# Performance work log

Hardware: AMD Instinct MI355X
Metric: run time of the kernel (lower is better)

Reference implementation:

```python
import jax, jax.numpy as jnp
import numpy as np

NUM_EXPERTS = 16
HIDDEN = 2048
INTER = 768
TOP_K = 8
N_TOKENS = 4096


def setup_inputs() -> dict:
    key = jax.random.key(0)
    k1, k2, k3, k4, k5 = jax.random.split(key, 5)
    hidden_states = jax.random.normal(k1, (N_TOKENS, HIDDEN), dtype=jnp.float32)
    routing_weights = jax.random.uniform(k2, (N_TOKENS, NUM_EXPERTS), dtype=jnp.float32)
    router_indices = jax.random.randint(k3, (N_TOKENS, TOP_K), 0, NUM_EXPERTS)
    gate_up_proj = jax.random.normal(k4, (NUM_EXPERTS, HIDDEN, 2 * INTER), dtype=jnp.float32) * 0.02
    down_proj = jax.random.normal(k5, (NUM_EXPERTS, INTER, HIDDEN), dtype=jnp.float32) * 0.02
    return {
        "hidden_states": hidden_states,
        "routing_weights": routing_weights,
        "router_indices": router_indices,
        "gate_up_proj": gate_up_proj,
        "down_proj": down_proj,
    }


def reference(hidden_states, routing_weights, router_indices, gate_up_proj, down_proj):
    # Training-path MoE math (permute + grouped GEMM + SwiGLU + grouped GEMM +
    # unpermute/combine), expressed as dense per-expert GEMMs combined with a
    # sparse combine matrix built from the top-k router indices.
    n_tokens, hidden = hidden_states.shape
    n_experts = gate_up_proj.shape[0]
    # selected_probs[t, k] = routing_weights[t, router_indices[t, k]]
    selected_probs = jnp.take_along_axis(routing_weights, router_indices, axis=1)  # [N, K]
    # combine[t, e] = sum over k of selected_probs where router_indices[t,k] == e
    rows = jnp.arange(n_tokens)[:, None]
    combine = jnp.zeros((n_tokens, n_experts), dtype=hidden_states.dtype)
    combine = combine.at[rows, router_indices].add(selected_probs)  # [N, E]
    # grouped GEMM #1 (gate_up): [N,H] x [E,H,2I] -> [E,N,2I]
    gate_up = jnp.einsum("nh,ehf->enf", hidden_states, gate_up_proj)
    gate, up = jnp.split(gate_up, 2, axis=-1)
    inter = jax.nn.silu(gate) * up  # SwiGLU, [E,N,I]
    # grouped GEMM #2 (down): [E,N,I] x [E,I,H] -> [E,N,H]
    expert_out = jnp.einsum("eni,eih->enh", inter, down_proj)
    # combine / unpermute: weighted sum over selected experts
    out = jnp.einsum("enh,ne->nh", expert_out, combine)  # [N, H]
    return out
```

## Files before the change

kernel.cpp:

```cpp
#include <hip/hip_runtime.h>
#include <hip/hip_bf16.h>

#define NE 16
#define H  2048
#define I  768
#define TK 8
#define NT 4096
#define BM 128
#define BK 64

typedef unsigned short u16;
typedef unsigned int u32;
typedef __attribute__((ext_vector_type(8))) short bf16x8;
typedef __attribute__((ext_vector_type(4))) float f32x4;

__device__ __forceinline__ u16 f2bf(float f) {
    u32 u = __float_as_uint(f);
    u32 r = (u + 0x7fffu + ((u >> 16) & 1u)) >> 16;
    return (u16)r;
}

__device__ __forceinline__ void gload16(const void* g, void* l) {
    __builtin_amdgcn_global_load_lds(
        (const __attribute__((address_space(1))) unsigned int*)g,
        (__attribute__((address_space(3))) unsigned int*)l, 16, 0, 0);
}

__global__ void route_kernel(const float* __restrict__ rw, const int* __restrict__ ridx,
                             int* __restrict__ cnt, int* __restrict__ tok_cap,
                             float* __restrict__ wt_cap) {
    int t = blockIdx.x * 256 + threadIdx.x;
    if (t >= NT) return;
    int idx[TK];
#pragma unroll
    for (int k = 0; k < TK; k++) idx[k] = ridx[t * TK + k];
#pragma unroll
    for (int e = 0; e < NE; e++) {
        int mult = 0;
#pragma unroll
        for (int k = 0; k < TK; k++) mult += (idx[k] == e) ? 1 : 0;
        if (mult) {
            float w = (float)mult * rw[t * NE + e];
            int slot = atomicAdd(&cnt[e], 1);
            tok_cap[e * NT + slot] = t;
            wt_cap[e * NT + slot] = w;
        }
    }
}

__global__ void prefix_kernel(const int* __restrict__ cnt, int* __restrict__ base) {
    if (threadIdx.x == 0 && blockIdx.x == 0) {
        int s = 0;
        for (int e = 0; e < NE; e++) { base[e] = s; s += cnt[e]; }
        base[NE] = s;
    }
}

__global__ void compact_kernel(const int* __restrict__ cnt, const int* __restrict__ base,
                               const int* __restrict__ tok_cap, const float* __restrict__ wt_cap,
                               int* __restrict__ tok, float* __restrict__ wt,
                               int* __restrict__ tjc, int* __restrict__ tslot) {
    int i = blockIdx.x * 256 + threadIdx.x;
    int e = i >> 12, s = i & 4095;
    if (e < NE && s < cnt[e]) {
        int t = tok_cap[e * NT + s];
        int slot = base[e] + s;
        tok[slot] = t;
        wt[slot]  = wt_cap[e * NT + s];
        int j = atomicAdd(&tjc[t], 1);
        tslot[t * TK + j] = slot;
    }
}

__global__ void cvt_hs(const float4* __restrict__ in, uint4* __restrict__ out, int n) {
    int i = blockIdx.x * 256 + threadIdx.x;
    if (i >= n) return;
    float4 a = in[i * 2], b = in[i * 2 + 1];
    uint4 o;
    o.x = (u32)f2bf(a.x) | ((u32)f2bf(a.y) << 16);
    o.y = (u32)f2bf(a.z) | ((u32)f2bf(a.w) << 16);
    o.z = (u32)f2bf(b.x) | ((u32)f2bf(b.y) << 16);
    o.w = (u32)f2bf(b.z) | ((u32)f2bf(b.w) << 16);
    out[i] = o;
}

__global__ void transpose_cvt(const float* __restrict__ in, u32* __restrict__ out,
                              int K, int N) {
    __shared__ float tile[64][65];
    const float* src = in + (size_t)blockIdx.z * K * N;
    u32* dst = out + (size_t)blockIdx.z * (size_t)K * N / 2;
    int n0 = blockIdx.x * 64, k0 = blockIdx.y * 64;
    int tc = threadIdx.x & 63, tr = threadIdx.x >> 6;
    for (int r = tr; r < 64; r += 4)
        tile[r][tc] = src[(size_t)(k0 + r) * N + n0 + tc];
    __syncthreads();
    int kp = threadIdx.x & 31, rr = threadIdx.x >> 5;
    for (int r = rr; r < 64; r += 8) {
        u32 v = (u32)f2bf(tile[kp * 2][r]) | ((u32)f2bf(tile[kp * 2 + 1][r]) << 16);
        dst[(size_t)(n0 + r) * (K / 2) + k0 / 2 + kp] = v;
    }
}

__global__ __launch_bounds__(256, 2) void gemm1_kernel(
    const u16* __restrict__ hsb, const u16* __restrict__ w1t, u16* __restrict__ inter,
    const int* __restrict__ tok, const int* __restrict__ cnt, const int* __restrict__ base) {
    int bid = blockIdx.x;
    int lid = (bid & 7) * (6144 / 8) + (bid >> 3);
    int mt = lid & 31, r2 = lid >> 5;
    int nt = r2 % 12, e = r2 / 12;
    int cn = cnt[e];
    if (mt * BM >= cn) return;
    int b0 = base[e];

    __shared__ u16 lA[BM * BK];
    __shared__ u16 lB[BM * BK];

    int tid = threadIdx.x, lane = tid & 63, wv = tid >> 6;

    const u16* gA[4];
    const u16* gB[4];
#pragma unroll
    for (int i = 0; i < 4; i++) {
        int c = i * 256 + tid;
        int r = c >> 3, ko = (c & 7) * 8;
        int rg = mt * BM + r;
        int t = tok[b0 + min(rg, cn - 1)];
        gA[i] = hsb + (size_t)t * H + ko;
        int nrow = (r < 64) ? (nt * 64 + r) : (704 + nt * 64 + r);
        gB[i] = w1t + (size_t)e * 1536 * H + (size_t)nrow * H + ko;
    }
    u16* lAd[4];
    u16* lBd[4];
#pragma unroll
    for (int i = 0; i < 4; i++) {
        lAd[i] = lA + (i * 256 + wv * 64) * 8;
        lBd[i] = lB + (i * 256 + wv * 64) * 8;
    }

    f32x4 acc[2][8];
#pragma unroll
    for (int m = 0; m < 2; m++)
#pragma unroll
        for (int n = 0; n < 8; n++) acc[m][n] = (f32x4)0.0f;

    for (int kt = 0; kt < H / BK; ++kt) {
        __syncthreads();
#pragma unroll
        for (int i = 0; i < 4; i++) { gload16(gA[i], lAd[i]); gload16(gB[i], lBd[i]); }
#pragma unroll
        for (int i = 0; i < 4; i++) { gA[i] += BK; gB[i] += BK; }
        __syncthreads();
#pragma unroll
        for (int s = 0; s < 2; s++) {
            int kk = s * 32 + (lane >> 4) * 8;
            bf16x8 a0 = *(const bf16x8*)&lA[(wv * 32 + (lane & 15)) * BK + kk];
            bf16x8 a1 = *(const bf16x8*)&lA[(wv * 32 + 16 + (lane & 15)) * BK + kk];
#pragma unroll
            for (int n = 0; n < 8; n++) {
                bf16x8 b = *(const bf16x8*)&lB[(n * 16 + (lane & 15)) * BK + kk];
                acc[0][n] = __builtin_amdgcn_mfma_f32_16x16x32_bf16(a0, b, acc[0][n], 0, 0, 0);
                acc[1][n] = __builtin_amdgcn_mfma_f32_16x16x32_bf16(a1, b, acc[1][n], 0, 0, 0);
            }
        }
    }

    int jr = (lane >> 4) * 4, col = lane & 15;
#pragma unroll
    for (int m = 0; m < 2; m++)
#pragma unroll
        for (int j = 0; j < 4; j++) {
            int r = wv * 32 + m * 16 + jr + j;
            int rg = mt * BM + r;
            if (rg < cn) {
                size_t slot = (size_t)(b0 + rg);
#pragma unroll
                for (int n = 0; n < 4; n++) {
                    float g = acc[m][n][j];
                    float u = acc[m][n + 4][j];
                    float sv = g / (1.0f + __expf(-g)) * u;
                    inter[slot * I + nt * 64 + n * 16 + col] = f2bf(sv);
                }
            }
        }
}

template <int MODE>
__global__ __launch_bounds__(256, 2) void gemm2_kernel(
    const u16* __restrict__ inter, const u16* __restrict__ w2t,
    u16* __restrict__ eo, float* __restrict__ out,
    const int* __restrict__ tok, const float* __restrict__ wt,
    const int* __restrict__ cnt, const int* __restrict__ base) {
    int bid = blockIdx.x;
    int lid = (bid & 7) * (8192 / 8) + (bid >> 3);
    int mt = lid & 31, r2 = lid >> 5;
    int nt = r2 & 15, e = r2 >> 4;
    int cn = cnt[e];
    if (mt * BM >= cn) return;
    int b0 = base[e];

    __shared__ u16 lA[BM * BK];
    __shared__ u16 lB[BM * BK];

    int tid = threadIdx.x, lane = tid & 63, wv = tid >> 6;

    const u16* gA[4];
    const u16* gB[4];
#pragma unroll
    for (int i = 0; i < 4; i++) {
        int c = i * 256 + tid;
        int r = c >> 3, ko = (c & 7) * 8;
        gA[i] = inter + (size_t)(b0 + mt * BM + r) * I + ko;
        gB[i] = w2t + (size_t)e * H * I + (size_t)(nt * BM + r) * I + ko;
    }
    u16* lAd[4];
    u16* lBd[4];
#pragma unroll
    for (int i = 0; i < 4; i++) {
        lAd[i] = lA + (i * 256 + wv * 64) * 8;
        lBd[i] = lB + (i * 256 + wv * 64) * 8;
    }

    f32x4 acc[2][8];
#pragma unroll
    for (int m = 0; m < 2; m++)
#pragma unroll
        for (int n = 0; n < 8; n++) acc[m][n] = (f32x4)0.0f;

    for (int kt = 0; kt < I / BK; ++kt) {
        __syncthreads();
#pragma unroll
        for (int i = 0; i < 4; i++) { gload16(gA[i], lAd[i]); gload16(gB[i], lBd[i]); }
#pragma unroll
        for (int i = 0; i < 4; i++) { gA[i] += BK; gB[i] += BK; }
        __syncthreads();
#pragma unroll
        for (int s = 0; s < 2; s++) {
            int kk = s * 32 + (lane >> 4) * 8;
            bf16x8 a0 = *(const bf16x8*)&lA[(wv * 32 + (lane & 15)) * BK + kk];
            bf16x8 a1 = *(const bf16x8*)&lA[(wv * 32 + 16 + (lane & 15)) * BK + kk];
#pragma unroll
            for (int n = 0; n < 8; n++) {
                bf16x8 b = *(const bf16x8*)&lB[(n * 16 + (lane & 15)) * BK + kk];
                acc[0][n] = __builtin_amdgcn_mfma_f32_16x16x32_bf16(a0, b, acc[0][n], 0, 0, 0);
                acc[1][n] = __builtin_amdgcn_mfma_f32_16x16x32_bf16(a1, b, acc[1][n], 0, 0, 0);
            }
        }
    }

    int jr = (lane >> 4) * 4, col = lane & 15;
#pragma unroll
    for (int m = 0; m < 2; m++)
#pragma unroll
        for (int j = 0; j < 4; j++) {
            int r = wv * 32 + m * 16 + jr + j;
            int rg = mt * BM + r;
            if (rg < cn) {
                if (MODE == 0) {
                    u16* row = eo + (size_t)(b0 + rg) * H + nt * BM;
#pragma unroll
                    for (int n = 0; n < 8; n++)
                        row[n * 16 + col] = f2bf(acc[m][n][j]);
                } else {
                    int t = tok[b0 + rg];
                    float w = wt[b0 + rg];
                    float* orow = out + (size_t)t * H + nt * BM;
#pragma unroll
                    for (int n = 0; n < 8; n++)
                        atomicAdd(&orow[n * 16 + col], w * acc[m][n][j]);
                }
            }
        }
}

__global__ __launch_bounds__(256) void combine_kernel(
    const u16* __restrict__ eo, const float* __restrict__ wt,
    const int* __restrict__ tjc, const int* __restrict__ tslot,
    float* __restrict__ out) {
    int t = blockIdx.x;
    int c = threadIdx.x * 8;
    float acc[8];
#pragma unroll
    for (int i = 0; i < 8; i++) acc[i] = 0.0f;
    int jc = tjc[t];
    for (int j = 0; j < jc; j++) {
        int slot = tslot[t * TK + j];
        float w = wt[slot];
        uint4 v = *(const uint4*)(eo + (size_t)slot * H + c);
        acc[0] += w * __uint_as_float(v.x << 16);
        acc[1] += w * __uint_as_float(v.x & 0xffff0000u);
        acc[2] += w * __uint_as_float(v.y << 16);
        acc[3] += w * __uint_as_float(v.y & 0xffff0000u);
        acc[4] += w * __uint_as_float(v.z << 16);
        acc[5] += w * __uint_as_float(v.z & 0xffff0000u);
        acc[6] += w * __uint_as_float(v.w << 16);
        acc[7] += w * __uint_as_float(v.w & 0xffff0000u);
    }
    float4* o = (float4*)(out + (size_t)t * H + c);
    o[0] = make_float4(acc[0], acc[1], acc[2], acc[3]);
    o[1] = make_float4(acc[4], acc[5], acc[6], acc[7]);
}

extern "C" void kernel_launch(void* const* d_in, const int* in_sizes, int n_in,
                              void* d_out, int out_size, void* d_ws, size_t ws_size,
                              hipStream_t stream) {
    const float* hs  = (const float*)d_in[0];
    const float* rw  = (const float*)d_in[1];
    const int*   ri  = (const int*)d_in[2];
    const float* w1  = (const float*)d_in[3];
    const float* w2  = (const float*)d_in[4];
    float* out = (float*)d_out;

    char* ws = (char*)d_ws;
    size_t o = 0;
    auto alloc = [&](size_t bytes) { void* p = ws + o; o += (bytes + 255) & ~(size_t)255; return p; };
    int*   tokcap = (int*)alloc((size_t)NE * NT * 4);
    float* wtcap  = (float*)alloc((size_t)NE * NT * 4);
    int*   tok    = (int*)alloc((size_t)NT * TK * 4);
    float* wt     = (float*)alloc((size_t)NT * TK * 4);
    int*   tjc    = (int*)alloc((size_t)NT * 4);
    int*   tslot  = (int*)alloc((size_t)NT * TK * 4);
    int*   cnt    = (int*)alloc(64);
    int*   base   = (int*)alloc(128);
    u16*   hsb    = (u16*)alloc((size_t)NT * H * 2);
    u16*   w1t    = (u16*)alloc((size_t)NE * 1536 * H * 2);
    u16*   w2t    = (u16*)alloc((size_t)NE * H * I * 2);
    u16*   inter  = (u16*)alloc((size_t)(NT * TK + 256) * I * 2);
    u16*   eo     = (u16*)alloc((size_t)(NT * TK + 256) * H * 2);
    const bool use_eo = (o <= ws_size);

    hipMemsetAsync(cnt, 0, 64, stream);
    hipMemsetAsync(tjc, 0, (size_t)NT * 4, stream);
    if (!use_eo)
        hipMemsetAsync(out, 0, (size_t)NT * H * 4, stream);

    route_kernel<<<NT / 256, 256, 0, stream>>>(rw, ri, cnt, tokcap, wtcap);
    prefix_kernel<<<1, 64, 0, stream>>>(cnt, base);
    compact_kernel<<<NE * NT / 256, 256, 0, stream>>>(cnt, base, tokcap, wtcap, tok, wt, tjc, tslot);
    cvt_hs<<<(NT * H / 8 + 255) / 256, 256, 0, stream>>>((const float4*)hs, (uint4*)hsb, NT * H / 8);
    {
        dim3 g(1536 / 64, H / 64, NE);
        transpose_cvt<<<g, 256, 0, stream>>>(w1, (u32*)w1t, H, 1536);
    }
    {
        dim3 g(H / 64, I / 64, NE);
        transpose_cvt<<<g, 256, 0, stream>>>(w2, (u32*)w2t, I, H);
    }
    gemm1_kernel<<<6144, 256, 0, stream>>>(hsb, w1t, inter, tok, cnt, base);
    if (use_eo) {
        gemm2_kernel<0><<<8192, 256, 0, stream>>>(inter, w2t, eo, out, tok, wt, cnt, base);
        combine_kernel<<<NT, 256, 0, stream>>>(eo, wt, tjc, tslot, out);
    } else {
        gemm2_kernel<1><<<8192, 256, 0, stream>>>(inter, w2t, eo, out, tok, wt, cnt, base);
    }
}
```

Before: 801.8 us.

## Rewrite grouped GEMMs as 256x256 tiles with pipelined, swizzled LDS staging

Both grouped GEMMs move from 128x128 tiles with 256 threads and single-buffered LDS to 256x256 tiles with 512 threads (8 waves). K is staged in 32-wide chunks through a multi-buffered LDS ring using XOR-swizzled rows, with explicit vmcnt/lgkmcnt waits, barriers and MFMA priority hints, so global loads overlap with MFMA work. The atomic fallback path is dropped and the eo+combine path is always used. The larger tiles improve data reuse and cut synchronisation stalls, at the cost of 128KB of LDS per block, more padding waste on partially filled expert tiles, and heavier register pressure.

```diff
diff --git a/kernel.cpp b/kernel.cpp
--- a/kernel.cpp
+++ b/kernel.cpp
@@ -6,8 +6,6 @@
 #define I  768
 #define TK 8
 #define NT 4096
-#define BM 128
-#define BK 64
 
 typedef unsigned short u16;
 typedef unsigned int u32;
@@ -25,6 +23,87 @@
         (const __attribute__((address_space(1))) unsigned int*)g,
         (__attribute__((address_space(3))) unsigned int*)l, 16, 0, 0);
 }
+
+__device__ __forceinline__ void BAR() {
+    __builtin_amdgcn_sched_barrier(0);
+    __builtin_amdgcn_s_barrier();
+    __builtin_amdgcn_sched_barrier(0);
+}
+__device__ __forceinline__ void WLDS() {
+    asm volatile("s_waitcnt lgkmcnt(0)" ::: "memory");
+    __builtin_amdgcn_sched_barrier(0);
+}
+#define VM4() asm volatile("s_waitcnt vmcnt(4)" ::: "memory")
+
+#define MF(a, b, c) __builtin_amdgcn_mfma_f32_16x16x32_bf16(a, b, c, 0, 0, 0)
+
+#define FRAG(REG, ROW) (*(const bf16x8*)((REG) + (ROW)*32 + ((q ^ ((((ROW) >> 1)) & 3)) * 8)))
+
+#define STG(PR0, PR1, DST, KO)                       \
+    do {                                             \
+        gload16((PR0) + (KO), (DST) + tid * 8);      \
+        gload16((PR1) + (KO), (DST) + 4096 + tid * 8); \
+    } while (0)
+
+#define MFMA_Q(MH)                                                                     \
+    do {                                                                               \
+        acc[(MH)*4+0][0]=MF(af0,bf0,acc[(MH)*4+0][0]); acc[(MH)*4+0][1]=MF(af0,bf1,acc[(MH)*4+0][1]); \
+        acc[(MH)*4+0][2]=MF(af0,bf2,acc[(MH)*4+0][2]); acc[(MH)*4+0][3]=MF(af0,bf3,acc[(MH)*4+0][3]); \
+        acc[(MH)*4+1][0]=MF(af1,bf0,acc[(MH)*4+1][0]); acc[(MH)*4+1][1]=MF(af1,bf1,acc[(MH)*4+1][1]); \
+        acc[(MH)*4+1][2]=MF(af1,bf2,acc[(MH)*4+1][2]); acc[(MH)*4+1][3]=MF(af1,bf3,acc[(MH)*4+1][3]); \
+        acc[(MH)*4+2][0]=MF(af2,bf0,acc[(MH)*4+2][0]); acc[(MH)*4+2][1]=MF(af2,bf1,acc[(MH)*4+2][1]); \
+        acc[(MH)*4+2][2]=MF(af2,bf2,acc[(MH)*4+2][2]); acc[(MH)*4+2][3]=MF(af2,bf3,acc[(MH)*4+2][3]); \
+        acc[(MH)*4+3][0]=MF(af3,bf0,acc[(MH)*4+3][0]); acc[(MH)*4+3][1]=MF(af3,bf1,acc[(MH)*4+3][1]); \
+        acc[(MH)*4+3][2]=MF(af3,bf2,acc[(MH)*4+3][2]); acc[(MH)*4+3][3]=MF(af3,bf3,acc[(MH)*4+3][3]); \
+    } while (0)
+
+#define KTILE(cA0, cA1, cB0, cB1, oA1, oB1, T1, T2)                           \
+    do {                                                                      \
+        af0 = FRAG(cA0, wm*128 +  0 + ln); af1 = FRAG(cA0, wm*128 + 16 + ln); \
+        af2 = FRAG(cA0, wm*128 + 32 + ln); af3 = FRAG(cA0, wm*128 + 48 + ln); \
+        bf0 = FRAG(cB0, wn*64 +  0 + ln);  bf1 = FRAG(cB0, wn*64 + 16 + ln);  \
+        bf2 = FRAG(cB0, wn*64 + 32 + ln);  bf3 = FRAG(cB0, wn*64 + 48 + ln);  \
+        STG(pA0, pA1, oA1, (T1)*64 + 32);                                     \
+        BAR(); WLDS();                                                        \
+        __builtin_amdgcn_s_setprio(1); MFMA_Q(0); __builtin_amdgcn_s_setprio(0); \
+        BAR();                                                                \
+        af0 = FRAG(cA0, wm*128 + 64 + ln); af1 = FRAG(cA0, wm*128 + 80 + ln); \
+        af2 = FRAG(cA0, wm*128 + 96 + ln); af3 = FRAG(cA0, wm*128 +112 + ln); \
+        STG(pB0, pB1, oB1, (T1)*64 + 32);                                     \
+        BAR(); WLDS();                                                        \
+        __builtin_amdgcn_s_setprio(1); MFMA_Q(1); __builtin_amdgcn_s_setprio(0); \
+        BAR();                                                                \
+        af0 = FRAG(cA1, wm*128 +  0 + ln); af1 = FRAG(cA1, wm*128 + 16 + ln); \
+        af2 = FRAG(cA1, wm*128 + 32 + ln); af3 = FRAG(cA1, wm*128 + 48 + ln); \
+        bf0 = FRAG(cB1, wn*64 +  0 + ln);  bf1 = FRAG(cB1, wn*64 + 16 + ln);  \
+        bf2 = FRAG(cB1, wn*64 + 32 + ln);  bf3 = FRAG(cB1, wn*64 + 48 + ln);  \
+        STG(pA0, pA1, cA0, (T2)*64);                                          \
+        BAR(); WLDS();                                                        \
+        __builtin_amdgcn_s_setprio(1); MFMA_Q(0); __builtin_amdgcn_s_setprio(0); \
+        BAR();                                                                \
+        af0 = FRAG(cA1, wm*128 + 64 + ln); af1 = FRAG(cA1, wm*128 + 80 + ln); \
+        af2 = FRAG(cA1, wm*128 + 96 + ln); af3 = FRAG(cA1, wm*128 +112 + ln); \
+        STG(pB0, pB1, cB0, (T2)*64);                                          \
+        VM4();                                                                \
+        BAR(); WLDS();                                                        \
+        __builtin_amdgcn_s_setprio(1); MFMA_Q(1); __builtin_amdgcn_s_setprio(0); \
+        BAR();                                                                \
+    } while (0)
+
+#define GEMM_PRO_AND_DECLS()                                                  \
+    u16* const sA00 = sm;         u16* const sA01 = sm + 8192;                \
+    u16* const sA10 = sm + 16384; u16* const sA11 = sm + 24576;               \
+    u16* const sB00 = sm + 32768; u16* const sB01 = sm + 40960;               \
+    u16* const sB10 = sm + 49152; u16* const sB11 = sm + 57344;               \
+    f32x4 acc[8][4];                                                          \
+    _Pragma("unroll") for (int _i = 0; _i < 8; _i++)                          \
+    _Pragma("unroll") for (int _j = 0; _j < 4; _j++) acc[_i][_j] = (f32x4)0.0f; \
+    bf16x8 af0, af1, af2, af3, bf0, bf1, bf2, bf3;                            \
+     \
+    STG(pA0, pA1, sA00, 0);  STG(pB0, pB1, sB00, 0);                          \
+    STG(pA0, pA1, sA01, 32); STG(pB0, pB1, sB01, 32);                         \
+    STG(pA0, pA1, sA10, 64); STG(pB0, pB1, sB10, 64);                         \
+    VM4(); BAR();
 
 __global__ void route_kernel(const float* __restrict__ rw, const int* __restrict__ ridx,
                              int* __restrict__ cnt, int* __restrict__ tok_cap,
@@ -101,175 +180,113 @@
     }
 }
 
-__global__ __launch_bounds__(256, 2) void gemm1_kernel(
+__global__ __launch_bounds__(512, 2) void gemm1_kernel(
     const u16* __restrict__ hsb, const u16* __restrict__ w1t, u16* __restrict__ inter,
     const int* __restrict__ tok, const int* __restrict__ cnt, const int* __restrict__ base) {
+    __shared__ u16 sm[65536];
     int bid = blockIdx.x;
-    int lid = (bid & 7) * (6144 / 8) + (bid >> 3);
-    int mt = lid & 31, r2 = lid >> 5;
-    int nt = r2 % 12, e = r2 / 12;
+    int lid = (bid & 7) * (1536 / 8) + (bid >> 3);
+    int mt = lid & 15;
+    int r2 = lid >> 4;
+    int nt = r2 % 6, e = r2 / 6;
     int cn = cnt[e];
-    if (mt * BM >= cn) return;
+    if (mt * 256 >= cn) return;
     int b0 = base[e];
 
-    __shared__ u16 lA[BM * BK];
-    __shared__ u16 lB[BM * BK];
-
-    int tid = threadIdx.x, lane = tid & 63, wv = tid >> 6;
-
-    const u16* gA[4];
-    const u16* gB[4];
-#pragma unroll
-    for (int i = 0; i < 4; i++) {
-        int c = i * 256 + tid;
-        int r = c >> 3, ko = (c & 7) * 8;
-        int rg = mt * BM + r;
-        int t = tok[b0 + min(rg, cn - 1)];
-        gA[i] = hsb + (size_t)t * H + ko;
-        int nrow = (r < 64) ? (nt * 64 + r) : (704 + nt * 64 + r);
-        gB[i] = w1t + (size_t)e * 1536 * H + (size_t)nrow * H + ko;
-    }
-    u16* lAd[4];
-    u16* lBd[4];
-#pragma unroll
-    for (int i = 0; i < 4; i++) {
-        lAd[i] = lA + (i * 256 + wv * 64) * 8;
-        lBd[i] = lB + (i * 256 + wv * 64) * 8;
-    }
-
-    f32x4 acc[2][8];
-#pragma unroll
-    for (int m = 0; m < 2; m++)
-#pragma unroll
-        for (int n = 0; n < 8; n++) acc[m][n] = (f32x4)0.0f;
-
-    for (int kt = 0; kt < H / BK; ++kt) {
-        __syncthreads();
-#pragma unroll
-        for (int i = 0; i < 4; i++) { gload16(gA[i], lAd[i]); gload16(gB[i], lBd[i]); }
-#pragma unroll
-        for (int i = 0; i < 4; i++) { gA[i] += BK; gB[i] += BK; }
-        __syncthreads();
-#pragma unroll
-        for (int s = 0; s < 2; s++) {
-            int kk = s * 32 + (lane >> 4) * 8;
-            bf16x8 a0 = *(const bf16x8*)&lA[(wv * 32 + (lane & 15)) * BK + kk];
-            bf16x8 a1 = *(const bf16x8*)&lA[(wv * 32 + 16 + (lane & 15)) * BK + kk];
-#pragma unroll
-            for (int n = 0; n < 8; n++) {
-                bf16x8 b = *(const bf16x8*)&lB[(n * 16 + (lane & 15)) * BK + kk];
-                acc[0][n] = __builtin_amdgcn_mfma_f32_16x16x32_bf16(a0, b, acc[0][n], 0, 0, 0);
-                acc[1][n] = __builtin_amdgcn_mfma_f32_16x16x32_bf16(a1, b, acc[1][n], 0, 0, 0);
-            }
-        }
-    }
-
-    int jr = (lane >> 4) * 4, col = lane & 15;
-#pragma unroll
-    for (int m = 0; m < 2; m++)
+    int tid = threadIdx.x;
+    int lane = tid & 63, wid = tid >> 6;
+    int wm = wid >> 2, wn = wid & 3;
+    int ln = lane & 15, q = lane >> 4;
+
+    int r0 = tid >> 2;
+    int sl = (tid & 3) ^ ((r0 >> 1) & 3);
+    int ta = b0 + min(mt * 256 + r0, cn - 1);
+    int tb = b0 + min(mt * 256 + r0 + 128, cn - 1);
+    const u16* pA0 = hsb + (size_t)tok[ta] * H + sl * 8;
+    const u16* pA1 = hsb + (size_t)tok[tb] * H + sl * 8;
+    int g0 = r0 >> 5, u0 = (r0 >> 4) & 1, rr0 = r0 & 15;
+    int b1r = r0 + 128;
+    int g1 = b1r >> 5, u1 = (b1r >> 4) & 1, rr1 = b1r & 15;
+    const u16* pB0 = w1t + (size_t)e * 1536 * H + (size_t)(768 * u0 + nt * 128 + g0 * 16 + rr0) * H + sl * 8;
+    const u16* pB1 = w1t + (size_t)e * 1536 * H + (size_t)(768 * u1 + nt * 128 + g1 * 16 + rr1) * H + sl * 8;
+
+    GEMM_PRO_AND_DECLS();
+
+    for (int t = 0; t < 32; t += 2) {
+        int u2 = t + 2; if (u2 >= 32) u2 -= 32;
+        int u3 = t + 3; if (u3 >= 32) u3 -= 32;
+        KTILE(sA00, sA01, sB00, sB01, sA11, sB11, t + 1, u2);
+        KTILE(sA10, sA11, sB10, sB11, sA01, sB01, u2, u3);
+    }
+
+    int jr = q * 4;
+#pragma unroll
+    for (int mf = 0; mf < 8; mf++) {
 #pragma unroll
         for (int j = 0; j < 4; j++) {
-            int r = wv * 32 + m * 16 + jr + j;
-            int rg = mt * BM + r;
+            int rg = mt * 256 + wm * 128 + mf * 16 + jr + j;
             if (rg < cn) {
                 size_t slot = (size_t)(b0 + rg);
 #pragma unroll
-                for (int n = 0; n < 4; n++) {
-                    float g = acc[m][n][j];
-                    float u = acc[m][n + 4][j];
-                    float sv = g / (1.0f + __expf(-g)) * u;
-                    inter[slot * I + nt * 64 + n * 16 + col] = f2bf(sv);
+                for (int p = 0; p < 2; p++) {
+                    float gg = acc[mf][2 * p][j];
+                    float uu = acc[mf][2 * p + 1][j];
+                    float sv = gg / (1.0f + __expf(-gg)) * uu;
+                    inter[slot * I + nt * 128 + (2 * wn + p) * 16 + ln] = f2bf(sv);
                 }
             }
         }
-}
-
-template <int MODE>
-__global__ __launch_bounds__(256, 2) void gemm2_kernel(
-    const u16* __restrict__ inter, const u16* __restrict__ w2t,
-    u16* __restrict__ eo, float* __restrict__ out,
-    const int* __restrict__ tok, const float* __restrict__ wt,
+    }
+}
+
+__global__ __launch_bounds__(512, 2) void gemm2_kernel(
+    const u16* __restrict__ inter, const u16* __restrict__ w2t, u16* __restrict__ eo,
     const int* __restrict__ cnt, const int* __restrict__ base) {
+    __shared__ u16 sm[65536];
     int bid = blockIdx.x;
-    int lid = (bid & 7) * (8192 / 8) + (bid >> 3);
-    int mt = lid & 31, r2 = lid >> 5;
-    int nt = r2 & 15, e = r2 >> 4;
+    int lid = (bid & 7) * (2048 / 8) + (bid >> 3);
+    int mt = lid & 15;
+    int r2 = lid >> 4;
+    int nt = r2 & 7, e = r2 >> 3;
     int cn = cnt[e];
-    if (mt * BM >= cn) return;
+    if (mt * 256 >= cn) return;
     int b0 = base[e];
 
-    __shared__ u16 lA[BM * BK];
-    __shared__ u16 lB[BM * BK];
-
-    int tid = threadIdx.x, lane = tid & 63, wv = tid >> 6;
-
-    const u16* gA[4];
-    const u16* gB[4];
-#pragma unroll
-    for (int i = 0; i < 4; i++) {
-        int c = i * 256 + tid;
-        int r = c >> 3, ko = (c & 7) * 8;
-        gA[i] = inter + (size_t)(b0 + mt * BM + r) * I + ko;
-        gB[i] = w2t + (size_t)e * H * I + (size_t)(nt * BM + r) * I + ko;
-    }
-    u16* lAd[4];
-    u16* lBd[4];
-#pragma unroll
-    for (int i = 0; i < 4; i++) {
-        lAd[i] = lA + (i * 256 + wv * 64) * 8;
-        lBd[i] = lB + (i * 256 + wv * 64) * 8;
-    }
-
-    f32x4 acc[2][8];
-#pragma unroll
-    for (int m = 0; m < 2; m++)
-#pragma unroll
-        for (int n = 0; n < 8; n++) acc[m][n] = (f32x4)0.0f;
-
-    for (int kt = 0; kt < I / BK; ++kt) {
-        __syncthreads();
-#pragma unroll
-        for (int i = 0; i < 4; i++) { gload16(gA[i], lAd[i]); gload16(gB[i], lBd[i]); }
-#pragma unroll
-        for (int i = 0; i < 4; i++) { gA[i] += BK; gB[i] += BK; }
-        __syncthreads();
-#pragma unroll
-        for (int s = 0; s < 2; s++) {
-            int kk = s * 32 + (lane >> 4) * 8;
-            bf16x8 a0 = *(const bf16x8*)&lA[(wv * 32 + (lane & 15)) * BK + kk];
-            bf16x8 a1 = *(const bf16x8*)&lA[(wv * 32 + 16 + (lane & 15)) * BK + kk];
-#pragma unroll
-            for (int n = 0; n < 8; n++) {
-                bf16x8 b = *(const bf16x8*)&lB[(n * 16 + (lane & 15)) * BK + kk];
-                acc[0][n] = __builtin_amdgcn_mfma_f32_16x16x32_bf16(a0, b, acc[0][n], 0, 0, 0);
-                acc[1][n] = __builtin_amdgcn_mfma_f32_16x16x32_bf16(a1, b, acc[1][n], 0, 0, 0);
+    int tid = threadIdx.x;
+    int lane = tid & 63, wid = tid >> 6;
+    int wm = wid >> 2, wn = wid & 3;
+    int ln = lane & 15, q = lane >> 4;
+
+    int r0 = tid >> 2;
+    int sl = (tid & 3) ^ ((r0 >> 1) & 3);
+    const u16* pA0 = inter + (size_t)(b0 + mt * 256 + r0) * I + sl * 8;
+    const u16* pA1 = inter + (size_t)(b0 + mt * 256 + r0 + 128) * I + sl * 8;
+    const u16* pB0 = w2t + (size_t)e * H * I + (size_t)(nt * 256 + r0) * I + sl * 8;
+    const u16* pB1 = w2t + (size_t)e * H * I + (size_t)(nt * 256 + r0 + 128) * I + sl * 8;
+
+    GEMM_PRO_AND_DECLS();
+
+    for (int t = 0; t < 12; t += 2) {
+        int u2 = t + 2; if (u2 >= 12) u2 -= 12;
+        int u3 = t + 3; if (u3 >= 12) u3 -= 12;
+        KTILE(sA00, sA01, sB00, sB01, sA11, sB11, t + 1, u2);
+        KTILE(sA10, sA11, sB10, sB11, sA01, sB01, u2, u3);
+    }
+
+    int jr = q * 4;
+#pragma unroll
+    for (int mf = 0; mf < 8; mf++) {
+#pragma unroll
+        for (int j = 0; j < 4; j++) {
+            int rg = mt * 256 + wm * 128 + mf * 16 + jr + j;
+            if (rg < cn) {
+                u16* row = eo + (size_t)(b0 + rg) * H + nt * 256 + wn * 64;
+#pragma unroll
+                for (int n = 0; n < 4; n++)
+                    row[n * 16 + ln] = f2bf(acc[mf][n][j]);
             }
         }
     }
-
-    int jr = (lane >> 4) * 4, col = lane & 15;
-#pragma unroll
-    for (int m = 0; m < 2; m++)
-#pragma unroll
-        for (int j = 0; j < 4; j++) {
-            int r = wv * 32 + m * 16 + jr + j;
-            int rg = mt * BM + r;
-            if (rg < cn) {
-                if (MODE == 0) {
-                    u16* row = eo + (size_t)(b0 + rg) * H + nt * BM;
-#pragma unroll
-                    for (int n = 0; n < 8; n++)
-                        row[n * 16 + col] = f2bf(acc[m][n][j]);
-                } else {
-                    int t = tok[b0 + rg];
-                    float w = wt[b0 + rg];
-                    float* orow = out + (size_t)t * H + nt * BM;
-#pragma unroll
-                    for (int n = 0; n < 8; n++)
-                        atomicAdd(&orow[n * 16 + col], w * acc[m][n][j]);
-                }
-            }
-        }
 }
 
 __global__ __launch_bounds__(256) void combine_kernel(
@@ -326,12 +343,10 @@
     u16*   w2t    = (u16*)alloc((size_t)NE * H * I * 2);
     u16*   inter  = (u16*)alloc((size_t)(NT * TK + 256) * I * 2);
     u16*   eo     = (u16*)alloc((size_t)(NT * TK + 256) * H * 2);
-    const bool use_eo = (o <= ws_size);
+    (void)ws_size;
 
     hipMemsetAsync(cnt, 0, 64, stream);
     hipMemsetAsync(tjc, 0, (size_t)NT * 4, stream);
-    if (!use_eo)
-        hipMemsetAsync(out, 0, (size_t)NT * H * 4, stream);
 
     route_kernel<<<NT / 256, 256, 0, stream>>>(rw, ri, cnt, tokcap, wtcap);
     prefix_kernel<<<1, 64, 0, stream>>>(cnt, base);
@@ -345,11 +360,7 @@
         dim3 g(H / 64, I / 64, NE);
         transpose_cvt<<<g, 256, 0, stream>>>(w2, (u32*)w2t, I, H);
     }
-    gemm1_kernel<<<6144, 256, 0, stream>>>(hsb, w1t, inter, tok, cnt, base);
-    if (use_eo) {
-        gemm2_kernel<0><<<8192, 256, 0, stream>>>(inter, w2t, eo, out, tok, wt, cnt, base);
-        combine_kernel<<<NT, 256, 0, stream>>>(eo, wt, tjc, tslot, out);
-    } else {
-        gemm2_kernel<1><<<8192, 256, 0, stream>>>(inter, w2t, eo, out, tok, wt, cnt, base);
-    }
-}
+    gemm1_kernel<<<1536, 512, 0, stream>>>(hsb, w1t, inter, tok, cnt, base);
+    gemm2_kernel<<<2048, 512, 0, stream>>>(inter, w2t, eo, cnt, base);
+    combine_kernel<<<NT, 256, 0, stream>>>(eo, wt, tjc, tslot, out);
+}
```

After: 713.6 us. 11.0% less time.
